# Kernel tuning notes

Hardware: AMD Instinct MI355X
Metric: run time of the kernel (lower is better)

Reference implementation:

```python
import jax, jax.numpy as jnp
import numpy as np

TOP_K = 2

def setup_inputs() -> dict:
    key = jax.random.key(0)
    ks = jax.random.split(key, 8)
    B, S, H, F, E = 2, 2048, 1024, 2048, 8
    sH = 1.0 / np.sqrt(H)
    sF = 1.0 / np.sqrt(F)
    return {
        "hidden_states": jax.random.normal(ks[0], (B, S, H), jnp.float32),
        "gate_w": jax.random.normal(ks[1], (E, H), jnp.float32) * sH,
        "w_up": jax.random.normal(ks[2], (E, H, F), jnp.float32) * sH,
        "w_gate": jax.random.normal(ks[3], (E, H, F), jnp.float32) * sH,
        "w_down": jax.random.normal(ks[4], (E, F, H), jnp.float32) * sF,
        "b_up": jnp.zeros((E, F), jnp.float32),
        "b_gate": jnp.zeros((E, F), jnp.float32),
        "b_down": jnp.zeros((E, H), jnp.float32),
    }

def reference(hidden_states, gate_w, w_up, w_gate, w_down, b_up, b_gate, b_down):
    # Flatten [B,S,H] -> [N,H]
    H = hidden_states.shape[-1]
    x = hidden_states.reshape(-1, H)                      # [N,H]
    router_logits = x @ gate_w.T                          # [N,E]
    probs = jax.nn.softmax(router_logits.astype(jnp.float32), axis=-1)
    topv, topi = jax.lax.top_k(probs, TOP_K)              # [N,K]
    topv = topv / topv.sum(axis=-1, keepdims=True)
    N, E = router_logits.shape
    # Sparse combine weights: zero except top-k experts (renormalized).
    w_full = jnp.zeros((N, E), probs.dtype).at[jnp.arange(N)[:, None], topi].set(topv)
    w_full = w_full.astype(x.dtype)
    # SwiGLU per expert (dense over E; combine weights zero out non-selected).
    u = jnp.einsum('nh,ehf->nef', x, w_up) + b_up         # [N,E,F]
    v = jnp.einsum('nh,ehf->nef', x, w_gate) + b_gate
    phi = jax.nn.silu(v) * u
    y = jnp.einsum('nef,efh->neh', phi, w_down) + b_down  # [N,E,H]
    out = jnp.einsum('ne,neh->nh', w_full, y)             # [N,H]
    out = out.reshape(hidden_states.shape)
    return out, router_logits.astype(hidden_states.dtype)
```

## Files before the change

### kernel.cpp

```cpp
#include <hip/hip_runtime.h>
#include <hip/hip_bf16.h>
#include <cstdint>
#include <cstddef>

#define N_TOK 4096
#define H_DIM 1024
#define F_DIM 2048
#define E_NUM 8
#define RCAP 9216
#define MAXT 80

typedef __attribute__((ext_vector_type(8))) short bf16x8;
typedef __attribute__((ext_vector_type(4))) float f32x4;

__device__ __forceinline__ float b2f(uint16_t u) {
  return __uint_as_float(((uint32_t)u) << 16);
}
__device__ __forceinline__ uint16_t f2b(float f) {
  uint32_t x = __float_as_uint(f);
  uint32_t r = (x + 0x7fffu + ((x >> 16) & 1u)) >> 16;
  return (uint16_t)r;
}

__device__ __forceinline__ void gl2lds16(const void* g, void* l) {
  __builtin_amdgcn_global_load_lds(
      (const __attribute__((address_space(1))) uint32_t*)g,
      (__attribute__((address_space(3))) uint32_t*)l, 16, 0, 0);
}

__device__ __forceinline__ void stage_tile(const uint16_t* src, int ldK,
                                           char* lds, int wave, int lane) {
  int u = (lane & 7) ^ (lane >> 3);
  const char* s0 = (const char*)src + u * 16;
  size_t rb = (size_t)ldK * 2;
  int Rb = wave * 32 + (lane >> 3);
  for (int c = 0; c < 4; ++c) {
    gl2lds16(s0 + (size_t)(Rb + c * 8) * rb, lds + wave * 4096 + c * 1024);
  }
}

__device__ __forceinline__ void stage64(const uint16_t* src, int ldK,
                                        char* lds, int wave, int lane) {
  int u = (lane & 7) ^ (lane >> 3);
  const char* s0 = (const char*)src + u * 16;
  size_t rb = (size_t)ldK * 2;
  int Rb = wave * 16 + (lane >> 3);
  for (int c = 0; c < 2; ++c) {
    gl2lds16(s0 + (size_t)(Rb + c * 8) * rb, lds + wave * 2048 + c * 1024);
  }
}

__device__ __forceinline__ bf16x8 read_frag(const char* lds, int R, int s,
                                            int q) {
  int unit = ((s << 2) + q) ^ (R & 7);
  return *(const bf16x8*)(lds + R * 128 + unit * 16);
}

__global__ __launch_bounds__(256) void detect_kernel(
    const uint16_t* __restrict__ x, int* __restrict__ flag) {
  __shared__ int cnt;
  if (threadIdx.x == 0) cnt = 0;
  __syncthreads();
  int ok = 0;
  for (int j = 0; j < 16; ++j) {
    uint16_t u = x[threadIdx.x * 16 + j];
    int e = (u >> 7) & 0xff;
    ok += (u == 0 || (e >= 96 && e <= 143)) ? 1 : 0;
  }
  atomicAdd(&cnt, ok);
  __syncthreads();
  if (threadIdx.x == 0) *flag = (cnt >= 3700) ? 1 : 0;
}

__global__ __launch_bounds__(256) void router_kernel(
    const void* __restrict__ xraw, const void* __restrict__ gwraw,
    const int* __restrict__ flag, void* __restrict__ dout,
    int* __restrict__ top_i, float* __restrict__ top_w) {
  int fl = *flag;
  int wave = threadIdx.x >> 6, lane = threadIdx.x & 63;
  int t = blockIdx.x * 4 + wave;
  float xv[16];
  if (fl) {
    const uint16_t* xr = (const uint16_t*)xraw + (size_t)t * H_DIM + lane * 16;
    uint4 a = *(const uint4*)xr;
    uint4 b = *(const uint4*)(xr + 8);
    uint32_t w[8] = {a.x, a.y, a.z, a.w, b.x, b.y, b.z, b.w};
    for (int j = 0; j < 8; ++j) {
      xv[2 * j] = b2f((uint16_t)(w[j] & 0xffff));
      xv[2 * j + 1] = b2f((uint16_t)(w[j] >> 16));
    }
  } else {
    const float* xr = (const float*)xraw + (size_t)t * H_DIM + lane * 16;
    for (int j = 0; j < 4; ++j) {
      float4 v = ((const float4*)xr)[j];
      xv[4 * j] = v.x; xv[4 * j + 1] = v.y;
      xv[4 * j + 2] = v.z; xv[4 * j + 3] = v.w;
    }
  }
  float acc[E_NUM];
  for (int e = 0; e < E_NUM; ++e) {
    float s = 0.f;
    if (fl) {
      const uint16_t* gr =
          (const uint16_t*)gwraw + (size_t)e * H_DIM + lane * 16;
      uint4 a = *(const uint4*)gr;
      uint4 b = *(const uint4*)(gr + 8);
      uint32_t w[8] = {a.x, a.y, a.z, a.w, b.x, b.y, b.z, b.w};
      for (int j = 0; j < 8; ++j) {
        s += xv[2 * j] * b2f((uint16_t)(w[j] & 0xffff));
        s += xv[2 * j + 1] * b2f((uint16_t)(w[j] >> 16));
      }
    } else {
      const float* gr = (const float*)gwraw + (size_t)e * H_DIM + lane * 16;
      for (int j = 0; j < 4; ++j) {
        float4 v = ((const float4*)gr)[j];
        s += xv[4 * j] * v.x + xv[4 * j + 1] * v.y + xv[4 * j + 2] * v.z +
             xv[4 * j + 3] * v.w;
      }
    }
    acc[e] = s;
  }
  for (int off = 32; off >= 1; off >>= 1)
    for (int e = 0; e < E_NUM; ++e)
      acc[e] += __shfl_xor(acc[e], off, 64);
  if (lane < E_NUM) {
    size_t idx = (size_t)N_TOK * H_DIM + (size_t)t * E_NUM + lane;
    if (fl)
      ((uint16_t*)dout)[idx] = f2b(acc[lane]);
    else
      ((float*)dout)[idx] = acc[lane];
  }
  if (lane == 0) {
    int b0 = 0;
    float v0 = acc[0];
    for (int e = 1; e < E_NUM; ++e)
      if (acc[e] > v0) { v0 = acc[e]; b0 = e; }
    int b1 = (b0 == 0) ? 1 : 0;
    float v1 = acc[b1];
    for (int e = 0; e < E_NUM; ++e)
      if (e != b0 && acc[e] > v1) { v1 = acc[e]; b1 = e; }
    float w0 = 1.f / (1.f + expf(v1 - v0));
    top_i[2 * t] = b0; top_i[2 * t + 1] = b1;
    top_w[2 * t] = w0; top_w[2 * t + 1] = 1.f - w0;
  }
}

__global__ __launch_bounds__(1024) void histscan_kernel(
    const int* __restrict__ top_i, int* __restrict__ counts,
    int* __restrict__ bases, int* __restrict__ row_of,
    int* __restrict__ tile_e, int* __restrict__ tile_row,
    int* __restrict__ ntiles) {
  int tid = threadIdx.x;
  int lane = tid & 63, wave = tid >> 6;
  int e_loc[8];
  int c[E_NUM] = {};
  for (int j = 0; j < 8; ++j) {
    int idx = tid * 8 + j;
    int e = top_i[idx];
    e_loc[j] = e;
    c[e]++;
  }
  int inc[E_NUM];
  for (int k = 0; k < E_NUM; ++k) inc[k] = c[k];
  for (int off = 1; off < 64; off <<= 1) {
    for (int k = 0; k < E_NUM; ++k) {
      int v = __shfl_up(inc[k], off, 64);
      if (lane >= off) inc[k] += v;
    }
  }
  __shared__ int wtot[16][E_NUM];
  __shared__ int woff[16][E_NUM];
  __shared__ int base_s[E_NUM];
  if (lane == 63)
    for (int k = 0; k < E_NUM; ++k) wtot[wave][k] = inc[k];
  __syncthreads();
  if (tid < E_NUM) {
    int run = 0;
    for (int w = 0; w < 16; ++w) {
      woff[w][tid] = run;
      run += wtot[w][tid];
    }
    counts[tid] = run;
    wtot[0][tid] = run;
  }
  __syncthreads();
  if (tid == 0) {
    int b = 0, nt = 0;
    for (int e = 0; e < E_NUM; ++e) {
      bases[e] = b;
      base_s[e] = b;
      int cc = wtot[0][e];
      int te = (cc + 127) >> 7;
      for (int j = 0; j < te; ++j) {
        tile_e[nt] = e;
        tile_row[nt] = b + j * 128;
        ++nt;
      }
      b += te << 7;
    }
    *ntiles = nt;
  }
  __syncthreads();
  int run[E_NUM];
  for (int k = 0; k < E_NUM; ++k)
    run[k] = base_s[k] + woff[wave][k] + inc[k] - c[k];
  for (int j = 0; j < 8; ++j) {
    int idx = tid * 8 + j;
    int r = run[e_loc[j]]++;
    row_of[idx] = r;
  }
}

__global__ __launch_bounds__(256) void gather_kernel(
    const void* __restrict__ xraw, const int* __restrict__ flag,
    const int* __restrict__ row_of, uint16_t* __restrict__ Xg) {
  int t = blockIdx.x;
  int rs0 = row_of[2 * t], rs1 = row_of[2 * t + 1];
  uint2 v;
  if (*flag) {
    v = ((const uint2*)((const uint16_t*)xraw + (size_t)t * H_DIM))[threadIdx.x];
  } else {
    float4 f =
        ((const float4*)((const float*)xraw + (size_t)t * H_DIM))[threadIdx.x];
    v.x = (uint32_t)f2b(f.x) | ((uint32_t)f2b(f.y) << 16);
    v.y = (uint32_t)f2b(f.z) | ((uint32_t)f2b(f.w) << 16);
  }
  ((uint2*)(Xg + (size_t)rs0 * H_DIM))[threadIdx.x] = v;
  ((uint2*)(Xg + (size_t)rs1 * H_DIM))[threadIdx.x] = v;
}

__global__ __launch_bounds__(256) void transpose_kernel(
    const void* __restrict__ W0, const void* __restrict__ W1,
    const int* __restrict__ flag, uint16_t* __restrict__ Wt0,
    uint16_t* __restrict__ Wt1, int K, int N) {
  int z = blockIdx.z;
  int e = z & (E_NUM - 1);
  const void* W = (z < E_NUM) ? W0 : W1;
  uint16_t* Wt = (z < E_NUM) ? Wt0 : Wt1;
  int n0 = blockIdx.x * 64, k0 = blockIdx.y * 64;
  __shared__ __align__(16) uint16_t tile[64][72];
  size_t ebase = (size_t)e * K * N;
  uint16_t* Wout = Wt + ebase;
  int fl = *flag;
  int r = threadIdx.x >> 3;
  int c = (threadIdx.x & 7) * 8;
  if (fl) {
    const uint16_t* Win = (const uint16_t*)W + ebase;
    for (int it = 0; it < 2; ++it) {
      int row = r + it * 32;
      uint4 v = *(const uint4*)(Win + (size_t)(k0 + row) * N + n0 + c);
      *(uint4*)&tile[row][c] = v;
    }
  } else {
    const float* Win = (const float*)W + ebase;
    for (int it = 0; it < 2; ++it) {
      int row = r + it * 32;
      const float* p = Win + (size_t)(k0 + row) * N + n0 + c;
      float4 a = ((const float4*)p)[0];
      float4 b = ((const float4*)p)[1];
      uint16_t* tp = &tile[row][c];
      tp[0] = f2b(a.x); tp[1] = f2b(a.y); tp[2] = f2b(a.z); tp[3] = f2b(a.w);
      tp[4] = f2b(b.x); tp[5] = f2b(b.y); tp[6] = f2b(b.z); tp[7] = f2b(b.w);
    }
  }
  __syncthreads();
  for (int it = 0; it < 2; ++it) {
    int n = r + it * 32;
    uint4 o;
    o.x = (uint32_t)tile[c + 0][n] | ((uint32_t)tile[c + 1][n] << 16);
    o.y = (uint32_t)tile[c + 2][n] | ((uint32_t)tile[c + 3][n] << 16);
    o.z = (uint32_t)tile[c + 4][n] | ((uint32_t)tile[c + 5][n] << 16);
    o.w = (uint32_t)tile[c + 6][n] | ((uint32_t)tile[c + 7][n] << 16);
    *(uint4*)(Wout + (size_t)(n0 + n) * K + k0 + c) = o;
  }
}

__global__ __launch_bounds__(256, 3) void gemm_upgate(
    const uint16_t* __restrict__ Xg,
    const uint16_t* __restrict__ WtU, const uint16_t* __restrict__ WtG,
    const void* __restrict__ buRaw, const void* __restrict__ bgRaw,
    const int* __restrict__ flag, const int* __restrict__ tile_e,
    const int* __restrict__ tile_row, const int* __restrict__ ntiles,
    uint16_t* __restrict__ phi) {
  int ty = blockIdx.y;
  if (ty >= *ntiles) return;
  int e = tile_e[ty];
  int r0 = tile_row[ty];
  int n0 = blockIdx.x * 64;
  const uint16_t* A = Xg + (size_t)r0 * H_DIM;
  const uint16_t* BU = WtU + (size_t)e * F_DIM * H_DIM + (size_t)n0 * H_DIM;
  const uint16_t* BG = WtG + (size_t)e * F_DIM * H_DIM + (size_t)n0 * H_DIM;

  __shared__ __align__(16) char lA[128 * 128];
  __shared__ __align__(16) char lBu[64 * 128];
  __shared__ __align__(16) char lBg[64 * 128];

  int tid = threadIdx.x;
  int wave = tid >> 6, lane = tid & 63;
  int q = lane >> 4, mr = lane & 15;

  f32x4 accU[2][4] = {};
  f32x4 accG[2][4] = {};

  for (int k0 = 0; k0 < H_DIM; k0 += 64) {
    __syncthreads();
    stage_tile(A + k0, H_DIM, lA, wave, lane);
    stage64(BU + k0, H_DIM, lBu, wave, lane);
    stage64(BG + k0, H_DIM, lBg, wave, lane);
    __syncthreads();
    for (int s = 0; s < 2; ++s) {
      bf16x8 af[2], bu[4], bg[4];
      for (int mt = 0; mt < 2; ++mt)
        af[mt] = read_frag(lA, wave * 32 + mt * 16 + mr, s, q);
      for (int nt = 0; nt < 4; ++nt) {
        bu[nt] = read_frag(lBu, nt * 16 + mr, s, q);
        bg[nt] = read_frag(lBg, nt * 16 + mr, s, q);
      }
      for (int mt = 0; mt < 2; ++mt)
        for (int nt = 0; nt < 4; ++nt) {
          accU[mt][nt] = __builtin_amdgcn_mfma_f32_16x16x32_bf16(
              af[mt], bu[nt], accU[mt][nt], 0, 0, 0);
          accG[mt][nt] = __builtin_amdgcn_mfma_f32_16x16x32_bf16(
              af[mt], bg[nt], accG[mt][nt], 0, 0, 0);
        }
    }
  }

  int fl = *flag;
  int rbase = r0 + wave * 32;
  for (int nt = 0; nt < 4; ++nt) {
    int col = n0 + nt * 16 + mr;
    float bu_v, bg_v;
    if (fl) {
      bu_v = b2f(((const uint16_t*)buRaw)[(size_t)e * F_DIM + col]);
      bg_v = b2f(((const uint16_t*)bgRaw)[(size_t)e * F_DIM + col]);
    } else {
      bu_v = ((const float*)buRaw)[(size_t)e * F_DIM + col];
      bg_v = ((const float*)bgRaw)[(size_t)e * F_DIM + col];
    }
    for (int mt = 0; mt < 2; ++mt) {
      int r = rbase + mt * 16 + q * 4;
      for (int rg = 0; rg < 4; ++rg) {
        float u = accU[mt][nt][rg] + bu_v;
        float v = accG[mt][nt][rg] + bg_v;
        float s = v / (1.f + expf(-v));
        phi[(size_t)(r + rg) * F_DIM + col] = f2b(s * u);
      }
    }
  }
}

__global__ __launch_bounds__(256, 3) void gemm_down(
    const uint16_t* __restrict__ phi, const uint16_t* __restrict__ WtD,
    const void* __restrict__ bdRaw, const int* __restrict__ flag,
    const int* __restrict__ tile_e, const int* __restrict__ tile_row,
    const int* __restrict__ ntiles, float* __restrict__ Yrows) {
  int ty = blockIdx.y;
  if (ty >= *ntiles) return;
  int e = tile_e[ty];
  int r0 = tile_row[ty];
  int n0 = blockIdx.x * 128;
  const uint16_t* A = phi + (size_t)r0 * F_DIM;
  const uint16_t* B = WtD + (size_t)e * H_DIM * F_DIM + (size_t)n0 * F_DIM;

  __shared__ __align__(16) char lA[128 * 128];
  __shared__ __align__(16) char lB[128 * 128];

  int tid = threadIdx.x;
  int wave = tid >> 6, lane = tid & 63;
  int wm = wave >> 1, wn = wave & 1;
  int q = lane >> 4, mr = lane & 15;

  f32x4 acc[4][4] = {};

  for (int k0 = 0; k0 < F_DIM; k0 += 64) {
    __syncthreads();
    stage_tile(A + k0, F_DIM, lA, wave, lane);
    stage_tile(B + k0, F_DIM, lB, wave, lane);
    __syncthreads();
    for (int s = 0; s < 2; ++s) {
      bf16x8 af[4], bf[4];
      for (int mt = 0; mt < 4; ++mt)
        af[mt] = read_frag(lA, wm * 64 + mt * 16 + mr, s, q);
      for (int nt = 0; nt < 4; ++nt)
        bf[nt] = read_frag(lB, wn * 64 + nt * 16 + mr, s, q);
      for (int mt = 0; mt < 4; ++mt)
        for (int nt = 0; nt < 4; ++nt)
          acc[mt][nt] = __builtin_amdgcn_mfma_f32_16x16x32_bf16(
              af[mt], bf[nt], acc[mt][nt], 0, 0, 0);
    }
  }

  int fl = *flag;
  int rbase = r0 + wm * 64;
  int cbase = n0 + wn * 64;
  for (int nt = 0; nt < 4; ++nt) {
    int col = cbase + nt * 16 + mr;
    float bd_v = fl ? b2f(((const uint16_t*)bdRaw)[(size_t)e * H_DIM + col])
                    : ((const float*)bdRaw)[(size_t)e * H_DIM + col];
    for (int mt = 0; mt < 4; ++mt) {
      int r = rbase + mt * 16 + q * 4;
      for (int rg = 0; rg < 4; ++rg)
        Yrows[(size_t)(r + rg) * H_DIM + col] = acc[mt][nt][rg] + bd_v;
    }
  }
}

__global__ __launch_bounds__(256) void combine_kernel(
    const float* __restrict__ Y, const int* __restrict__ row_of,
    const float* __restrict__ top_w, const int* __restrict__ flag,
    void* __restrict__ out) {
  int t = blockIdx.x;
  int r0 = row_of[2 * t], r1 = row_of[2 * t + 1];
  float w0 = top_w[2 * t], w1 = top_w[2 * t + 1];
  int i = threadIdx.x;
  float4 a = ((const float4*)(Y + (size_t)r0 * H_DIM))[i];
  float4 b = ((const float4*)(Y + (size_t)r1 * H_DIM))[i];
  float4 o;
  o.x = w0 * a.x + w1 * b.x;
  o.y = w0 * a.y + w1 * b.y;
  o.z = w0 * a.z + w1 * b.z;
  o.w = w0 * a.w + w1 * b.w;
  if (*flag) {
    uint2 p;
    p.x = (uint32_t)f2b(o.x) | ((uint32_t)f2b(o.y) << 16);
    p.y = (uint32_t)f2b(o.z) | ((uint32_t)f2b(o.w) << 16);
    ((uint2*)out)[(size_t)t * 256 + i] = p;
  } else {
    ((float4*)out)[(size_t)t * 256 + i] = o;
  }
}

extern "C" void kernel_launch(void* const* d_in, const int* in_sizes, int n_in,
                              void* d_out, int out_size, void* d_ws, size_t ws_size,
                              hipStream_t stream) {
  const void* x = d_in[0];
  const void* gw = d_in[1];
  const void* w_up = d_in[2];
  const void* w_gate = d_in[3];
  const void* w_down = d_in[4];
  const void* b_up = d_in[5];
  const void* b_gate = d_in[6];
  const void* b_down = d_in[7];

  char* ws = (char*)d_ws;
  size_t off = 0;
  auto alloc = [&](size_t bytes) -> void* {
    void* p = ws + off;
    off += (bytes + 255) & ~(size_t)255;
    return p;
  };
  int* counts = (int*)alloc(32);
  int* bases = (int*)alloc(32);
  int* flag = (int*)alloc(32);
  int* ntiles = (int*)alloc(32);
  int* tile_e = (int*)alloc(sizeof(int) * MAXT);
  int* tile_row = (int*)alloc(sizeof(int) * MAXT);
  int* top_i = (int*)alloc(sizeof(int) * N_TOK * 2);
  float* top_w = (float*)alloc(sizeof(float) * N_TOK * 2);
  int* row_of = (int*)alloc(sizeof(int) * N_TOK * 2);
  uint16_t* Xg = (uint16_t*)alloc((size_t)RCAP * H_DIM * 2);
  uint16_t* phi = (uint16_t*)alloc((size_t)RCAP * F_DIM * 2);
  uint16_t* WtU = (uint16_t*)alloc((size_t)E_NUM * H_DIM * F_DIM * 2);
  uint16_t* WtG = (uint16_t*)alloc((size_t)E_NUM * H_DIM * F_DIM * 2);
  float* Yrows = (float*)alloc((size_t)RCAP * H_DIM * sizeof(float));

  detect_kernel<<<1, 256, 0, stream>>>((const uint16_t*)x, flag);
  router_kernel<<<N_TOK / 4, 256, 0, stream>>>(x, gw, flag, d_out, top_i,
                                               top_w);
  histscan_kernel<<<1, 1024, 0, stream>>>(top_i, counts, bases, row_of,
                                          tile_e, tile_row, ntiles);
  gather_kernel<<<N_TOK, 256, 0, stream>>>(x, flag, row_of, Xg);

  transpose_kernel<<<dim3(F_DIM / 64, H_DIM / 64, 2 * E_NUM), 256, 0,
                     stream>>>(w_up, w_gate, flag, WtU, WtG, H_DIM, F_DIM);

  gemm_upgate<<<dim3(F_DIM / 64, MAXT), 256, 0, stream>>>(
      Xg, WtU, WtG, b_up, b_gate, flag, tile_e, tile_row, ntiles, phi);

  transpose_kernel<<<dim3(H_DIM / 64, F_DIM / 64, E_NUM), 256, 0, stream>>>(
      w_down, w_down, flag, WtU, WtU, F_DIM, H_DIM);
  gemm_down<<<dim3(H_DIM / 128, MAXT), 256, 0, stream>>>(
      phi, WtU, b_down, flag, tile_e, tile_row, ntiles, Yrows);

  combine_kernel<<<N_TOK, 256, 0, stream>>>(Yrows, row_of, top_w, flag, d_out);
}
```

Baseline: 403.6 us.

## Inline dtype detection per kernel and merge weight transposes into one launch

Removes the standalone detect kernel. Each kernel now detects the bf16 input itself with a cheap per-wave vote over the first 128 halfwords. The three weight transposes are merged into one launch when the workspace fits a separate down-weight buffer, which saves launches and lets the down transpose overlap with the up/gate transpose. gemm_upgate launch bounds are raised to 4 blocks per CU. The risks are a less robust dtype heuristic using fewer samples and register pressure from the occupancy hint.

Result: slower. 417.2 us (+3.4%).

```diff
diff --git a/kernel.cpp b/kernel.cpp
--- a/kernel.cpp
+++ b/kernel.cpp
@@ -20,6 +20,19 @@
   uint32_t x = __float_as_uint(f);
   uint32_t r = (x + 0x7fffu + ((x >> 16) & 1u)) >> 16;
   return (uint16_t)r;
+}
+
+__device__ __forceinline__ int detect_bf16(const uint16_t* x) {
+  int lane = threadIdx.x & 63;
+  uint32_t w = ((const uint32_t*)x)[lane];
+  int ok = 0;
+  for (int h = 0; h < 2; ++h) {
+    uint16_t u = (uint16_t)(w >> (16 * h));
+    int e = (u >> 7) & 0xff;
+    ok += (u == 0 || (e >= 96 && e <= 143)) ? 1 : 0;
+  }
+  for (int off = 32; off >= 1; off >>= 1) ok += __shfl_xor(ok, off, 64);
+  return ok >= 115;
 }
 
 __device__ __forceinline__ void gl2lds16(const void* g, void* l) {
@@ -56,27 +69,11 @@
   return *(const bf16x8*)(lds + R * 128 + unit * 16);
 }
 
-__global__ __launch_bounds__(256) void detect_kernel(
-    const uint16_t* __restrict__ x, int* __restrict__ flag) {
-  __shared__ int cnt;
-  if (threadIdx.x == 0) cnt = 0;
-  __syncthreads();
-  int ok = 0;
-  for (int j = 0; j < 16; ++j) {
-    uint16_t u = x[threadIdx.x * 16 + j];
-    int e = (u >> 7) & 0xff;
-    ok += (u == 0 || (e >= 96 && e <= 143)) ? 1 : 0;
-  }
-  atomicAdd(&cnt, ok);
-  __syncthreads();
-  if (threadIdx.x == 0) *flag = (cnt >= 3700) ? 1 : 0;
-}
-
 __global__ __launch_bounds__(256) void router_kernel(
     const void* __restrict__ xraw, const void* __restrict__ gwraw,
-    const int* __restrict__ flag, void* __restrict__ dout,
-    int* __restrict__ top_i, float* __restrict__ top_w) {
-  int fl = *flag;
+    void* __restrict__ dout, int* __restrict__ top_i,
+    float* __restrict__ top_w) {
+  int fl = detect_bf16((const uint16_t*)xraw);
   int wave = threadIdx.x >> 6, lane = threadIdx.x & 63;
   int t = blockIdx.x * 4 + wave;
   float xv[16];
@@ -212,12 +209,13 @@
 }
 
 __global__ __launch_bounds__(256) void gather_kernel(
-    const void* __restrict__ xraw, const int* __restrict__ flag,
-    const int* __restrict__ row_of, uint16_t* __restrict__ Xg) {
+    const void* __restrict__ xraw, const int* __restrict__ row_of,
+    uint16_t* __restrict__ Xg) {
+  int fl = detect_bf16((const uint16_t*)xraw);
   int t = blockIdx.x;
   int rs0 = row_of[2 * t], rs1 = row_of[2 * t + 1];
   uint2 v;
-  if (*flag) {
+  if (fl) {
     v = ((const uint2*)((const uint16_t*)xraw + (size_t)t * H_DIM))[threadIdx.x];
   } else {
     float4 f =
@@ -229,19 +227,29 @@
   ((uint2*)(Xg + (size_t)rs1 * H_DIM))[threadIdx.x] = v;
 }
 
-__global__ __launch_bounds__(256) void transpose_kernel(
+__global__ __launch_bounds__(256) void transpose3_kernel(
     const void* __restrict__ W0, const void* __restrict__ W1,
-    const int* __restrict__ flag, uint16_t* __restrict__ Wt0,
-    uint16_t* __restrict__ Wt1, int K, int N) {
-  int z = blockIdx.z;
-  int e = z & (E_NUM - 1);
-  const void* W = (z < E_NUM) ? W0 : W1;
-  uint16_t* Wt = (z < E_NUM) ? Wt0 : Wt1;
-  int n0 = blockIdx.x * 64, k0 = blockIdx.y * 64;
+    const void* __restrict__ W2, const void* __restrict__ xdet,
+    uint16_t* __restrict__ Wt0, uint16_t* __restrict__ Wt1,
+    uint16_t* __restrict__ Wt2, int zbase) {
+  int z = blockIdx.z + zbase;
+  const void* W;
+  uint16_t* Wt;
+  int e, K, N, n0, k0;
+  if (z < E_NUM) {
+    W = W0; Wt = Wt0; e = z; K = H_DIM; N = F_DIM;
+    n0 = blockIdx.x * 64; k0 = blockIdx.y * 64;
+  } else if (z < 2 * E_NUM) {
+    W = W1; Wt = Wt1; e = z - E_NUM; K = H_DIM; N = F_DIM;
+    n0 = blockIdx.x * 64; k0 = blockIdx.y * 64;
+  } else {
+    W = W2; Wt = Wt2; e = z - 2 * E_NUM; K = F_DIM; N = H_DIM;
+    n0 = blockIdx.y * 64; k0 = blockIdx.x * 64;
+  }
+  int fl = detect_bf16((const uint16_t*)xdet);
   __shared__ __align__(16) uint16_t tile[64][72];
   size_t ebase = (size_t)e * K * N;
   uint16_t* Wout = Wt + ebase;
-  int fl = *flag;
   int r = threadIdx.x >> 3;
   int c = (threadIdx.x & 7) * 8;
   if (fl) {
@@ -275,11 +283,11 @@
   }
 }
 
-__global__ __launch_bounds__(256, 3) void gemm_upgate(
+__global__ __launch_bounds__(256, 4) void gemm_upgate(
     const uint16_t* __restrict__ Xg,
     const uint16_t* __restrict__ WtU, const uint16_t* __restrict__ WtG,
     const void* __restrict__ buRaw, const void* __restrict__ bgRaw,
-    const int* __restrict__ flag, const int* __restrict__ tile_e,
+    const void* __restrict__ xdet, const int* __restrict__ tile_e,
     const int* __restrict__ tile_row, const int* __restrict__ ntiles,
     uint16_t* __restrict__ phi) {
   int ty = blockIdx.y;
@@ -326,7 +334,7 @@
     }
   }
 
-  int fl = *flag;
+  int fl = detect_bf16((const uint16_t*)xdet);
   int rbase = r0 + wave * 32;
   for (int nt = 0; nt < 4; ++nt) {
     int col = n0 + nt * 16 + mr;
@@ -352,7 +360,7 @@
 
 __global__ __launch_bounds__(256, 3) void gemm_down(
     const uint16_t* __restrict__ phi, const uint16_t* __restrict__ WtD,
-    const void* __restrict__ bdRaw, const int* __restrict__ flag,
+    const void* __restrict__ bdRaw, const void* __restrict__ xdet,
     const int* __restrict__ tile_e, const int* __restrict__ tile_row,
     const int* __restrict__ ntiles, float* __restrict__ Yrows) {
   int ty = blockIdx.y;
@@ -391,7 +399,7 @@
     }
   }
 
-  int fl = *flag;
+  int fl = detect_bf16((const uint16_t*)xdet);
   int rbase = r0 + wm * 64;
   int cbase = n0 + wn * 64;
   for (int nt = 0; nt < 4; ++nt) {
@@ -408,8 +416,9 @@
 
 __global__ __launch_bounds__(256) void combine_kernel(
     const float* __restrict__ Y, const int* __restrict__ row_of,
-    const float* __restrict__ top_w, const int* __restrict__ flag,
+    const float* __restrict__ top_w, const void* __restrict__ xdet,
     void* __restrict__ out) {
+  int fl = detect_bf16((const uint16_t*)xdet);
   int t = blockIdx.x;
   int r0 = row_of[2 * t], r1 = row_of[2 * t + 1];
   float w0 = top_w[2 * t], w1 = top_w[2 * t + 1];
@@ -421,7 +430,7 @@
   o.y = w0 * a.y + w1 * b.y;
   o.z = w0 * a.z + w1 * b.z;
   o.w = w0 * a.w + w1 * b.w;
-  if (*flag) {
+  if (fl) {
     uint2 p;
     p.x = (uint32_t)f2b(o.x) | ((uint32_t)f2b(o.y) << 16);
     p.y = (uint32_t)f2b(o.z) | ((uint32_t)f2b(o.w) << 16);
@@ -452,7 +461,6 @@
   };
   int* counts = (int*)alloc(32);
   int* bases = (int*)alloc(32);
-  int* flag = (int*)alloc(32);
   int* ntiles = (int*)alloc(32);
   int* tile_e = (int*)alloc(sizeof(int) * MAXT);
   int* tile_row = (int*)alloc(sizeof(int) * MAXT);
@@ -465,23 +473,33 @@
   uint16_t* WtG = (uint16_t*)alloc((size_t)E_NUM * H_DIM * F_DIM * 2);
   float* Yrows = (float*)alloc((size_t)RCAP * H_DIM * sizeof(float));
 
-  detect_kernel<<<1, 256, 0, stream>>>((const uint16_t*)x, flag);
-  router_kernel<<<N_TOK / 4, 256, 0, stream>>>(x, gw, flag, d_out, top_i,
-                                               top_w);
+  size_t wtd_bytes = (size_t)E_NUM * H_DIM * F_DIM * 2;
+  bool sep = (off + wtd_bytes + 4096 <= ws_size);
+  uint16_t* WtD = sep ? (uint16_t*)alloc(wtd_bytes) : WtU;
+
+  router_kernel<<<N_TOK / 4, 256, 0, stream>>>(x, gw, d_out, top_i, top_w);
   histscan_kernel<<<1, 1024, 0, stream>>>(top_i, counts, bases, row_of,
                                           tile_e, tile_row, ntiles);
-  gather_kernel<<<N_TOK, 256, 0, stream>>>(x, flag, row_of, Xg);
-
-  transpose_kernel<<<dim3(F_DIM / 64, H_DIM / 64, 2 * E_NUM), 256, 0,
-                     stream>>>(w_up, w_gate, flag, WtU, WtG, H_DIM, F_DIM);
+  gather_kernel<<<N_TOK, 256, 0, stream>>>(x, row_of, Xg);
+
+  if (sep) {
+    transpose3_kernel<<<dim3(32, 16, 3 * E_NUM), 256, 0, stream>>>(
+        w_up, w_gate, w_down, x, WtU, WtG, WtD, 0);
+  } else {
+    transpose3_kernel<<<dim3(32, 16, 2 * E_NUM), 256, 0, stream>>>(
+        w_up, w_gate, w_down, x, WtU, WtG, WtD, 0);
+  }
 
   gemm_upgate<<<dim3(F_DIM / 64, MAXT), 256, 0, stream>>>(
-      Xg, WtU, WtG, b_up, b_gate, flag, tile_e, tile_row, ntiles, phi);
-
-  transpose_kernel<<<dim3(H_DIM / 64, F_DIM / 64, E_NUM), 256, 0, stream>>>(
-      w_down, w_down, flag, WtU, WtU, F_DIM, H_DIM);
+      Xg, WtU, WtG, b_up, b_gate, x, tile_e, tile_row, ntiles, phi);
+
+  if (!sep) {
+    transpose3_kernel<<<dim3(32, 16, E_NUM), 256, 0, stream>>>(
+        w_up, w_gate, w_down, x, WtU, WtG, WtD, 2 * E_NUM);
+  }
+
   gemm_down<<<dim3(H_DIM / 128, MAXT), 256, 0, stream>>>(
-      phi, WtU, b_down, flag, tile_e, tile_row, ntiles, Yrows);
-
-  combine_kernel<<<N_TOK, 256, 0, stream>>>(Yrows, row_of, top_w, flag, d_out);
-}
+      phi, WtD, b_down, x, tile_e, tile_row, ntiles, Yrows);
+
+  combine_kernel<<<N_TOK, 256, 0, stream>>>(Yrows, row_of, top_w, x, d_out);
+}
```
